# Performance work log

Hardware: AMD Instinct MI355X
Metric: run time of the kernel (lower is better)

## Reference

```python
import jax, jax.numpy as jnp
import numpy as np

KSIZE = 51  # radius=50 is even -> incremented to 51 in __init__


def _gaussian_1d(ksize):
    # cv2.getGaussianKernel with sigma<=0: sigma = 0.3*((ksize-1)*0.5 - 1) + 0.8
    sigma = 0.3 * ((ksize - 1) * 0.5 - 1) + 0.8
    x = np.arange(ksize, dtype=np.float64) - (ksize - 1) / 2
    g = np.exp(-(x * x) / (2.0 * sigma * sigma))
    g = g / g.sum()
    return g.astype(np.float32)


def _blur(img, kernel1d):
    """Separable Gaussian blur with reflect padding.
    Mathematically identical to the 2D conv with outer(g, g) in the torch code.
    img: (b, c, h, w), kernel1d: (k,)
    """
    k = kernel1d.shape[0]
    p = k // 2
    b, c, h, w = img.shape
    x = jnp.pad(img, ((0, 0), (0, 0), (p, p), (p, p)), mode='reflect')
    x = x.reshape(b * c, 1, h + 2 * p, w + 2 * p)
    # vertical pass then horizontal pass (conv vs correlation irrelevant: symmetric kernel)
    kv = kernel1d.reshape(1, 1, k, 1)
    kh = kernel1d.reshape(1, 1, 1, k)
    dn = ('NCHW', 'OIHW', 'NCHW')
    x = jax.lax.conv_general_dilated(x, kv, (1, 1), 'VALID', dimension_numbers=dn)
    x = jax.lax.conv_general_dilated(x, kh, (1, 1), 'VALID', dimension_numbers=dn)
    return x.reshape(b, c, h, w)


def setup_inputs() -> dict:
    key = jax.random.key(0)
    img = jax.random.uniform(key, (16, 3, 512, 512), dtype=jnp.float32)
    kernel1d = jnp.asarray(_gaussian_1d(KSIZE))
    return {"img": img, "kernel1d": kernel1d}


def reference(img, kernel1d):
    weight = 0.5
    threshold = 10.0
    blur = _blur(img, kernel1d)
    residual = img - blur
    mask = (jnp.abs(residual) * 255.0 > threshold).astype(img.dtype)
    soft_mask = _blur(mask, kernel1d)
    sharp = jnp.clip(img + weight * residual, 0.0, 1.0)
    return soft_mask * sharp + (1.0 - soft_mask) * img
```

## Files before the change

### kernel.cpp

```cpp
#include <hip/hip_runtime.h>
#include <hip/hip_bf16.h>


typedef __attribute__((ext_vector_type(8))) short bf16x8;
typedef __attribute__((ext_vector_type(4))) float f32x4;

constexpr int IMG = 512, NIMG = 48, K = 51;
constexpr int SP = 136;
constexpr int YP = 136;
constexpr int SROWS = 128;
constexpr int SDATA = 122;

__device__ __forceinline__ float bf2f(unsigned short u) {
    return __builtin_bit_cast(float, (unsigned)u << 16);
}
__device__ __forceinline__ unsigned short f2bf(float f) {
    unsigned u = __builtin_bit_cast(unsigned, f);
    u += 0x7FFF + ((u >> 16) & 1);
    return (unsigned short)(u >> 16);
}
__device__ __forceinline__ int refl(int i) {
    i = i < 0 ? -i : i;
    return i >= IMG ? 2 * IMG - 2 - i : i;
}

template <int PASS>
__global__ __launch_bounds__(512, 8) void usm_kern(const float* __restrict__ img,
                                                   unsigned short* __restrict__ resbuf,
                                                   unsigned char* __restrict__ maskbuf,
                                                   float* __restrict__ out,
                                                   const float* __restrict__ k1d) {
    __shared__ unsigned short st[SROWS * SP];
    unsigned short* const Hl = st;

    const int tid = threadIdx.x, lane = tid & 63;
    const int wv = __builtin_amdgcn_readfirstlane(tid >> 6);
    const int m16 = lane & 15, g = lane >> 4;

    const int id = blockIdx.x;
    const int sw = (id & 7) * 384 + (id >> 3);
    const int bz = sw >> 6, r6 = sw & 63, byy = r6 >> 3, bxx = r6 & 7;
    const int x0 = bxx * 64, y0 = byy * 64;
    const size_t base = (size_t)bz * (IMG * IMG);
    const float* __restrict__ imgb = img + base;
    unsigned short* __restrict__ resb = resbuf + base;
    unsigned char* __restrict__ maskb = maskbuf + base;
    float* __restrict__ outb = out + base;

    bf16x8 a_v[2], a_h[2];
#pragma unroll
    for (int rs = 0; rs < 2; ++rs) {
        float gt[9];
#pragma unroll
        for (int e = 0; e < 9; ++e) {
            const int t = 32 * rs + 8 * g + e - m16;
            gt[e] = ((unsigned)t < (unsigned)K) ? k1d[t] : 0.f;
        }
#pragma unroll
        for (int j = 0; j < 8; ++j) {
            a_v[rs][j] = (short)f2bf(gt[j]);
            a_h[rs][j] = (short)f2bf(gt[j + 1]);
        }
    }
    const float gg0 = k1d[0], gg49 = k1d[49], gg50 = k1d[50];

    const bool xedge = (bxx == 0) | (bxx == 7);
    const int r0t = tid >> 4, c8 = (tid & 15) * 8;
#pragma unroll
    for (int j = 0; j < 4; ++j) {
        const int s = r0t + 32 * j;
        const int rowo = refl(y0 - 33 + min(s, SDATA - 1)) * IMG + (x0 - 32 + c8);
        unsigned pk[4];
        if (PASS == 0) {
            float v[8];
            if (!xedge) {
                const f32x4 f0 = *(const f32x4*)&imgb[rowo];
                const f32x4 f1 = *(const f32x4*)&imgb[rowo + 4];
#pragma unroll
                for (int e = 0; e < 4; ++e) { v[e] = f0[e]; v[e + 4] = f1[e]; }
            } else {
                const int rb = rowo - (x0 - 32 + c8);
#pragma unroll
                for (int e = 0; e < 8; ++e) v[e] = imgb[rb + refl(x0 - 32 + c8 + e)];
            }
#pragma unroll
            for (int w = 0; w < 4; ++w)
                pk[w] = (unsigned)f2bf(v[2 * w]) | ((unsigned)f2bf(v[2 * w + 1]) << 16);
        } else {
            unsigned char mb[8];
            if (!xedge) {
                const uint2 mv = *(const uint2*)&maskb[rowo];
#pragma unroll
                for (int e = 0; e < 4; ++e) {
                    mb[e] = (unsigned char)(mv.x >> (8 * e));
                    mb[e + 4] = (unsigned char)(mv.y >> (8 * e));
                }
            } else {
                const int rb = rowo - (x0 - 32 + c8);
#pragma unroll
                for (int e = 0; e < 8; ++e) mb[e] = maskb[rb + refl(x0 - 32 + c8 + e)];
            }
#pragma unroll
            for (int w = 0; w < 4; ++w)
                pk[w] = (mb[2 * w] ? 0x3F80u : 0u) | ((mb[2 * w + 1] ? 0x3F80u : 0u) << 16);
        }
        *(uint4*)&st[s * SP + c8] = make_uint4(pk[0], pk[1], pk[2], pk[3]);
    }
    __syncthreads();

    f32x4 cacc[4];
#pragma unroll
    for (int k4 = 0; k4 < 4; ++k4) {
        const int t = wv + 8 * k4;
        const int xs = t & 3, yt = t >> 2;
        const int n = 16 * yt + m16;
        f32x4 acc = {0.f, 0.f, 0.f, 0.f};
#pragma unroll
        for (int rs = 0; rs < 2; ++rs) {
            const bf16x8 b = *(const bf16x8*)&st[n * SP + 16 * xs + 8 + 32 * rs + 8 * g];
            acc = __builtin_amdgcn_mfma_f32_16x16x32_bf16(a_h[rs], b, acc, 0, 0, 0);
        }
        if (g == 0) acc[0] = fmaf(gg0,  bf2f(st[n * SP + 16 * xs + 7]),  acc[0]);
        if (g == 3) acc[3] = fmaf(gg50, bf2f(st[n * SP + 16 * xs + 72]), acc[3]);
        cacc[k4] = acc;
    }
    __syncthreads();

#pragma unroll
    for (int k4 = 0; k4 < 4; ++k4) {
        const int t = wv + 8 * k4;
        const int xs = t & 3, yt = t >> 2;
        const int n = 16 * yt + m16;
#pragma unroll
        for (int q = 0; q < 4; ++q)
            Hl[(16 * xs + 4 * g + q) * YP + n] = f2bf(cacc[k4][q]);
    }
    __syncthreads();

#pragma unroll
    for (int k2 = 0; k2 < 2; ++k2) {
        const int t = wv + 8 * k2;
        const int xs2 = t & 3, ys = t >> 2;
        const int xl = 16 * xs2 + m16;
        f32x4 acc = {0.f, 0.f, 0.f, 0.f};
#pragma unroll
        for (int rs = 0; rs < 2; ++rs) {
            const bf16x8 b = *(const bf16x8*)&Hl[xl * YP + 16 * ys + 8 + 32 * rs + 8 * g];
            acc = __builtin_amdgcn_mfma_f32_16x16x32_bf16(a_v[rs], b, acc, 0, 0, 0);
        }
        if (g == 3) {
            const float h72 = bf2f(Hl[xl * YP + 16 * ys + 72]);
            const float h73 = bf2f(Hl[xl * YP + 16 * ys + 73]);
            acc[2] = fmaf(gg50, h72, acc[2]);
            acc[3] = fmaf(gg49, h72, fmaf(gg50, h73, acc[3]));
        }
        const int yl0 = 16 * ys + 4 * g;
#pragma unroll
        for (int q = 0; q < 4; ++q) {
            const int di = (y0 + yl0 + q) * IMG + (x0 + xl);
            const float iv = imgb[di];
            if (PASS == 0) {
                const float rv = iv - acc[q];
                resb[di] = f2bf(rv);
                maskb[di] = (fabsf(rv) * 255.0f > 10.0f) ? 1 : 0;
            } else {
                const float rv = bf2f(resb[di]);
                float sharp = fmaf(0.5f, rv, iv);
                sharp = fminf(fmaxf(sharp, 0.f), 1.f);
                outb[di] = fmaf(acc[q], sharp - iv, iv);
            }
        }
    }
}

extern "C" void kernel_launch(void* const* d_in, const int* in_sizes, int n_in,
                              void* d_out, int out_size, void* d_ws, size_t ws_size,
                              hipStream_t stream) {
    (void)in_sizes; (void)n_in; (void)out_size; (void)ws_size;
    const float* img = (const float*)d_in[0];
    const float* k1d = (const float*)d_in[1];
    float* out = (float*)d_out;
    unsigned short* rs = (unsigned short*)d_ws;
    unsigned char* mk = (unsigned char*)d_ws + (size_t)NIMG * IMG * IMG * 2;

    const dim3 grid(NIMG * 64);

    usm_kern<0><<<grid, 512, 0, stream>>>(img, rs, mk, out, k1d);
    usm_kern<1><<<grid, 512, 0, stream>>>(img, rs, mk, out, k1d);
}
```

Baseline: 96.42 us.

## Use taller 64x128 tiles, drop mask buffer, derive mask from bf16 residual

Tiles grow from 64x64 to 64 wide by 128 tall, which lowers the fraction of the vertical halo (50 rows) that has to be reloaded and recomputed per output. The separate byte mask buffer is removed: pass 1 rebuilds the mask by thresholding the stored bf16 residual with an integer compare, so one fewer global write stream and read stream is needed. Pass 0 now takes the image value from the bf16 tile already in shared memory instead of reloading the fp32 image from global memory. In exchange, LDS use per block goes up and the occupancy hint drops from 8 to 6. The residual and the mask threshold are now computed from bf16-rounded image values, which can flip mask pixels that sit near the threshold.

```diff
diff --git a/kernel.cpp b/kernel.cpp
--- a/kernel.cpp
+++ b/kernel.cpp
@@ -7,9 +7,9 @@
 
 constexpr int IMG = 512, NIMG = 48, K = 51;
 constexpr int SP = 136;
-constexpr int YP = 136;
-constexpr int SROWS = 128;
-constexpr int SDATA = 122;
+constexpr int YP = 200;
+constexpr int SROWS = 192;
+constexpr int SDATA = 186;
 
 __device__ __forceinline__ float bf2f(unsigned short u) {
     return __builtin_bit_cast(float, (unsigned)u << 16);
@@ -25,9 +25,8 @@
 }
 
 template <int PASS>
-__global__ __launch_bounds__(512, 8) void usm_kern(const float* __restrict__ img,
+__global__ __launch_bounds__(512, 6) void usm_kern(const float* __restrict__ img,
                                                    unsigned short* __restrict__ resbuf,
-                                                   unsigned char* __restrict__ maskbuf,
                                                    float* __restrict__ out,
                                                    const float* __restrict__ k1d) {
     __shared__ unsigned short st[SROWS * SP];
@@ -38,13 +37,12 @@
     const int m16 = lane & 15, g = lane >> 4;
 
     const int id = blockIdx.x;
-    const int sw = (id & 7) * 384 + (id >> 3);
-    const int bz = sw >> 6, r6 = sw & 63, byy = r6 >> 3, bxx = r6 & 7;
-    const int x0 = bxx * 64, y0 = byy * 64;
+    const int sw = (id & 7) * 192 + (id >> 3);
+    const int bz = sw >> 5, r5 = sw & 31, byy = r5 >> 3, bxx = r5 & 7;
+    const int x0 = bxx * 64, y0 = byy * 128;
     const size_t base = (size_t)bz * (IMG * IMG);
     const float* __restrict__ imgb = img + base;
     unsigned short* __restrict__ resb = resbuf + base;
-    unsigned char* __restrict__ maskb = maskbuf + base;
     float* __restrict__ outb = out + base;
 
     bf16x8 a_v[2], a_h[2];
@@ -67,7 +65,7 @@
     const bool xedge = (bxx == 0) | (bxx == 7);
     const int r0t = tid >> 4, c8 = (tid & 15) * 8;
 #pragma unroll
-    for (int j = 0; j < 4; ++j) {
+    for (int j = 0; j < 6; ++j) {
         const int s = r0t + 32 * j;
         const int rowo = refl(y0 - 33 + min(s, SDATA - 1)) * IMG + (x0 - 32 + c8);
         unsigned pk[4];
@@ -87,31 +85,34 @@
             for (int w = 0; w < 4; ++w)
                 pk[w] = (unsigned)f2bf(v[2 * w]) | ((unsigned)f2bf(v[2 * w + 1]) << 16);
         } else {
-            unsigned char mb[8];
+            unsigned rw[4];
             if (!xedge) {
-                const uint2 mv = *(const uint2*)&maskb[rowo];
-#pragma unroll
-                for (int e = 0; e < 4; ++e) {
-                    mb[e] = (unsigned char)(mv.x >> (8 * e));
-                    mb[e + 4] = (unsigned char)(mv.y >> (8 * e));
-                }
+                const uint4 q4 = *(const uint4*)&resb[rowo];
+                rw[0] = q4.x; rw[1] = q4.y; rw[2] = q4.z; rw[3] = q4.w;
             } else {
                 const int rb = rowo - (x0 - 32 + c8);
 #pragma unroll
-                for (int e = 0; e < 8; ++e) mb[e] = maskb[rb + refl(x0 - 32 + c8 + e)];
-            }
-#pragma unroll
-            for (int w = 0; w < 4; ++w)
-                pk[w] = (mb[2 * w] ? 0x3F80u : 0u) | ((mb[2 * w + 1] ? 0x3F80u : 0u) << 16);
+                for (int w = 0; w < 4; ++w) {
+                    const unsigned short e0 = resb[rb + refl(x0 - 32 + c8 + 2 * w)];
+                    const unsigned short e1 = resb[rb + refl(x0 - 32 + c8 + 2 * w + 1)];
+                    rw[w] = (unsigned)e0 | ((unsigned)e1 << 16);
+                }
+            }
+#pragma unroll
+            for (int w = 0; w < 4; ++w) {
+                const unsigned lo = ((rw[w] & 0x7FFFu) > 0x3D20u) ? 0x3F80u : 0u;
+                const unsigned hi = (((rw[w] >> 16) & 0x7FFFu) > 0x3D20u) ? 0x3F80u : 0u;
+                pk[w] = lo | (hi << 16);
+            }
         }
         *(uint4*)&st[s * SP + c8] = make_uint4(pk[0], pk[1], pk[2], pk[3]);
     }
     __syncthreads();
 
-    f32x4 cacc[4];
-#pragma unroll
-    for (int k4 = 0; k4 < 4; ++k4) {
-        const int t = wv + 8 * k4;
+    f32x4 cacc[6];
+#pragma unroll
+    for (int k6 = 0; k6 < 6; ++k6) {
+        const int t = wv + 8 * k6;
         const int xs = t & 3, yt = t >> 2;
         const int n = 16 * yt + m16;
         f32x4 acc = {0.f, 0.f, 0.f, 0.f};
@@ -122,24 +123,37 @@
         }
         if (g == 0) acc[0] = fmaf(gg0,  bf2f(st[n * SP + 16 * xs + 7]),  acc[0]);
         if (g == 3) acc[3] = fmaf(gg50, bf2f(st[n * SP + 16 * xs + 72]), acc[3]);
-        cacc[k4] = acc;
+        cacc[k6] = acc;
+    }
+
+    unsigned short civ[4][4];
+    if (PASS == 0) {
+#pragma unroll
+        for (int k4 = 0; k4 < 4; ++k4) {
+            const int t = wv + 8 * k4;
+            const int xs2 = t & 3, ys = t >> 2;
+            const int xl = 16 * xs2 + m16;
+#pragma unroll
+            for (int q = 0; q < 4; ++q)
+                civ[k4][q] = st[(33 + 16 * ys + 4 * g + q) * SP + xl + 32];
+        }
+    }
+    __syncthreads();
+
+#pragma unroll
+    for (int k6 = 0; k6 < 6; ++k6) {
+        const int t = wv + 8 * k6;
+        const int xs = t & 3, yt = t >> 2;
+        const int n = 16 * yt + m16;
+#pragma unroll
+        for (int q = 0; q < 4; ++q)
+            Hl[(16 * xs + 4 * g + q) * YP + n] = f2bf(cacc[k6][q]);
     }
     __syncthreads();
 
 #pragma unroll
     for (int k4 = 0; k4 < 4; ++k4) {
         const int t = wv + 8 * k4;
-        const int xs = t & 3, yt = t >> 2;
-        const int n = 16 * yt + m16;
-#pragma unroll
-        for (int q = 0; q < 4; ++q)
-            Hl[(16 * xs + 4 * g + q) * YP + n] = f2bf(cacc[k4][q]);
-    }
-    __syncthreads();
-
-#pragma unroll
-    for (int k2 = 0; k2 < 2; ++k2) {
-        const int t = wv + 8 * k2;
         const int xs2 = t & 3, ys = t >> 2;
         const int xl = 16 * xs2 + m16;
         f32x4 acc = {0.f, 0.f, 0.f, 0.f};
@@ -158,12 +172,11 @@
 #pragma unroll
         for (int q = 0; q < 4; ++q) {
             const int di = (y0 + yl0 + q) * IMG + (x0 + xl);
-            const float iv = imgb[di];
             if (PASS == 0) {
-                const float rv = iv - acc[q];
-                resb[di] = f2bf(rv);
-                maskb[di] = (fabsf(rv) * 255.0f > 10.0f) ? 1 : 0;
+                const float iv = bf2f(civ[k4][q]);
+                resb[di] = f2bf(iv - acc[q]);
             } else {
+                const float iv = imgb[di];
                 const float rv = bf2f(resb[di]);
                 float sharp = fmaf(0.5f, rv, iv);
                 sharp = fminf(fmaxf(sharp, 0.f), 1.f);
@@ -181,10 +194,9 @@
     const float* k1d = (const float*)d_in[1];
     float* out = (float*)d_out;
     unsigned short* rs = (unsigned short*)d_ws;
-    unsigned char* mk = (unsigned char*)d_ws + (size_t)NIMG * IMG * IMG * 2;
-
-    const dim3 grid(NIMG * 64);
-
-    usm_kern<0><<<grid, 512, 0, stream>>>(img, rs, mk, out, k1d);
-    usm_kern<1><<<grid, 512, 0, stream>>>(img, rs, mk, out, k1d);
-}
+
+    const dim3 grid(NIMG * 32);
+
+    usm_kern<0><<<grid, 512, 0, stream>>>(img, rs, out, k1d);
+    usm_kern<1><<<grid, 512, 0, stream>>>(img, rs, out, k1d);
+}
```

Result: faster. 91.68 us, median of 2 (-4.9%).
